# Kernel optimization log

Measured on AMD Instinct MI355X. Metric: run time of the kernel, lower is better.

Reference implementation:

```python
import jax, jax.numpy as jnp
import numpy as np

B, S, E, DQ, DV = 8, 2048, 1024, 128, 128


def setup_inputs() -> dict:
    k0 = jax.random.key(0)
    ks = jax.random.split(k0, 10)
    scale_in = 1.0 / np.sqrt(E)
    return {
        "pad_mask": jax.random.uniform(ks[0], (B, S)) < 0.1,  # True = padded key position
        "query": jax.random.normal(ks[1], (B, S, E), jnp.float32),
        "key": jax.random.normal(ks[2], (B, S, E), jnp.float32),
        "value": jax.random.normal(ks[3], (B, S, E), jnp.float32),
        "Wq": jax.random.uniform(ks[4], (E, DQ), jnp.float32, -scale_in, scale_in),
        "bq": jnp.zeros((DQ,), jnp.float32),
        "Wk": jax.random.uniform(ks[5], (E, DQ), jnp.float32, -scale_in, scale_in),
        "bk": jnp.zeros((DQ,), jnp.float32),
        "Wv": jax.random.uniform(ks[6], (E, DV), jnp.float32, -scale_in, scale_in),
        "bv": jnp.zeros((DV,), jnp.float32),
    }


def reference(pad_mask, query, key, value, Wq, bq, Wk, bk, Wv, bv):
    # Linear projections (torch Linear: x @ W^T + b; weights stored pre-transposed here)
    q = query @ Wq + bq  # [B,S,DQ]
    k = key @ Wk + bk    # [B,S,DQ]
    v = value @ Wv + bv  # [B,S,DV]

    scores = jnp.einsum("bqd,bkd->bqk", q, k)  # [B,S,S]
    # Causal mask applied BEFORE scaling (as in source); -inf/scale is still -inf
    seq = scores.shape[1]
    causal = jnp.triu(jnp.ones((seq, seq), bool), k=1)
    scores = jnp.where(causal[None], -jnp.inf, scores)
    scores = scores / jnp.asarray(q.shape[-1] ** 0.5, scores.dtype)
    # Padding mask: mask key positions with -1e9 (broadcast over query dim)
    scores = jnp.where(pad_mask[:, None, :], jnp.asarray(-1e9, scores.dtype), scores)

    attn = jax.nn.softmax(scores, axis=-1)
    return jnp.einsum("bqk,bkd->bqd", attn, v)  # [B,S,DV]
```

## Files before the change

### kernel.cpp

```cpp
#include <hip/hip_runtime.h>
#include <hip/hip_bf16.h>

#define SEQ 2048
#define EMB 1024
#define DH  128
#define QSCALE 0.08838834764831845f

typedef __attribute__((ext_vector_type(4))) float f32x4;
typedef __attribute__((ext_vector_type(8))) short bf16x8;
typedef __attribute__((ext_vector_type(4))) short bf16x4;

__device__ __forceinline__ short f2bf(float f) {
  unsigned u = __builtin_bit_cast(unsigned, f);
  u += 0x7fffu + ((u >> 16) & 1u);
  return (short)(u >> 16);
}

__device__ __forceinline__ float bf2f(short s) {
  unsigned u = ((unsigned)(unsigned short)s) << 16;
  return __builtin_bit_cast(float, u);
}

__device__ __forceinline__ f32x4 mfma16(bf16x8 a, bf16x8 b, f32x4 c) {
  return __builtin_amdgcn_mfma_f32_16x16x32_bf16(a, b, c, 0, 0, 0);
}

__device__ __forceinline__ void gl_lds16(void* lds_base, const void* gsrc) {
  __builtin_amdgcn_global_load_lds(
      (const __attribute__((address_space(1))) void*)gsrc,
      (__attribute__((address_space(3))) void*)lds_base, 16, 0, 0);
}

__global__ void prep_weights(const float* __restrict__ Wq, const float* __restrict__ Wk,
                             const float* __restrict__ Wv, short* __restrict__ wt) {
  int gid = blockIdx.x * 256 + threadIdx.x;
  int lane = gid & 63, c = lane & 15, g = (lane >> 4) & 3;
  int nb = (gid >> 6) & 7;
  int kk = (gid >> 9) & 31;
  int p = gid >> 14;
  const float* W = (p == 0) ? Wq : ((p == 1) ? Wk : Wv);
  bf16x8 v;
#pragma unroll
  for (int j = 0; j < 8; ++j)
    v[j] = f2bf(W[(kk * 32 + g * 8 + j) * DH + nb * 16 + c]);
  *(bf16x8*)(&wt[(size_t)gid * 8]) = v;
}

__global__ __launch_bounds__(256, 3) void proj_gemm(
    const float* __restrict__ Xq, const float* __restrict__ Xk, const float* __restrict__ Xv,
    const short* __restrict__ wt,
    const float* __restrict__ bq, const float* __restrict__ bk, const float* __restrict__ bv,
    short* __restrict__ qp, short* __restrict__ kp, short* __restrict__ vt) {
  const int tid = threadIdx.x;
  const int w = tid >> 6, lane = tid & 63;
  const int g = lane >> 4, c = lane & 15;
  const int p = blockIdx.x >> 8, mb = blockIdx.x & 255;
  const int row0 = (mb << 6) + (w << 4);
  const float* X    = (p == 0) ? Xq : ((p == 1) ? Xk : Xv);
  const float* bias = (p == 0) ? bq : ((p == 1) ? bk : bv);

  const f32x4* ap = (const f32x4*)(X + (size_t)(row0 + c) * 1024 + (g << 3));
  const bf16x8* wf = (const bf16x8*)(wt + ((size_t)p << 17)) + lane;

  f32x4 acc[8];
#pragma unroll
  for (int i = 0; i < 8; ++i) acc[i] = (f32x4){0.f, 0.f, 0.f, 0.f};

  f32x4 a0A, a1A, a0B, a1B;
  bf16x8 bA[8], bB[8];

  a0A = ap[0];
  a1A = ap[1];
#pragma unroll
  for (int nb = 0; nb < 8; ++nb) bA[nb] = wf[nb << 6];

#pragma unroll 1
  for (int kk = 0; kk < 32; kk += 2) {
    a0B = ap[(kk + 1) * 8];
    a1B = ap[(kk + 1) * 8 + 1];
#pragma unroll
    for (int nb = 0; nb < 8; ++nb) bB[nb] = wf[(kk + 1) * 512 + (nb << 6)];

    {
      bf16x8 a;
#pragma unroll
      for (int j = 0; j < 4; ++j) { a[j] = f2bf(a0A[j]); a[4 + j] = f2bf(a1A[j]); }
#pragma unroll
      for (int nb = 0; nb < 8; ++nb) acc[nb] = mfma16(a, bA[nb], acc[nb]);
    }

    if (kk + 2 < 32) {
      a0A = ap[(kk + 2) * 8];
      a1A = ap[(kk + 2) * 8 + 1];
#pragma unroll
      for (int nb = 0; nb < 8; ++nb) bA[nb] = wf[(kk + 2) * 512 + (nb << 6)];
    }

    {
      bf16x8 a;
#pragma unroll
      for (int j = 0; j < 4; ++j) { a[j] = f2bf(a0B[j]); a[4 + j] = f2bf(a1B[j]); }
#pragma unroll
      for (int nb = 0; nb < 8; ++nb) acc[nb] = mfma16(a, bB[nb], acc[nb]);
    }
  }

  float bvals[8];
#pragma unroll
  for (int nb = 0; nb < 8; ++nb) bvals[nb] = bias[nb * 16 + c];

  if (p < 2) {
    short* outp = (p == 0) ? qp : kp;
    float sc = (p == 0) ? QSCALE : 1.0f;
#pragma unroll
    for (int r = 0; r < 4; ++r) {
      int token = row0 + g * 4 + r;
#pragma unroll
      for (int nb = 0; nb < 8; ++nb)
        outp[token * 128 + nb * 16 + c] = f2bf((acc[nb][r] + bvals[nb]) * sc);
    }
  } else {
    int tok0 = row0 + g * 4;
    int b_ = tok0 >> 11, s_ = tok0 & 2047;
#pragma unroll
    for (int nb = 0; nb < 8; ++nb) {
      int col = nb * 16 + c;
      bf16x4 v4;
#pragma unroll
      for (int r = 0; r < 4; ++r) v4[r] = f2bf(acc[nb][r] + bvals[nb]);
      *(bf16x4*)(&vt[((size_t)(b_ * 128 + col)) * 2048 + s_]) = v4;
    }
  }
}

__global__ __launch_bounds__(256) void avgv2_kernel(
    const short* __restrict__ vt, const int* __restrict__ pad,
    const float* __restrict__ bvv, float* __restrict__ avgv) {
  int b = blockIdx.x >> 3, dg = blockIdx.x & 7;
  int t = threadIdx.x, doff = t >> 4, sl = t & 15;
  int d = dg * 16 + doff;
  const short* vrow = vt + ((size_t)(b * 128 + d)) * 2048 + sl * 128;
  const int* prow = pad + (b << 11) + sl * 128;
  float sum = 0.f;
  int cnt = 0;
  for (int i = 0; i < 16; ++i) {
    bf16x8 v8 = *(const bf16x8*)(vrow + i * 8);
#pragma unroll
    for (int j = 0; j < 8; ++j) {
      int pd = prow[i * 8 + j];
      cnt += (pd != 0);
      if (pd) sum += bf2f(v8[j]);
    }
  }
#pragma unroll
  for (int xm = 1; xm < 16; xm <<= 1) {
    sum += __shfl_xor(sum, xm, 64);
    cnt += __shfl_xor(cnt, xm, 64);
  }
  if (sl == 0) avgv[(b << 7) + d] = (cnt > 0) ? (sum / (float)cnt) : 0.f;
  (void)bvv;
}

__device__ __forceinline__ void stage_kv(short* kb, short* vb,
                                         const char* kb_base, const char* vb_base,
                                         int kt, int w, int lane) {
#pragma unroll
  for (int ch = w; ch < 16; ch += 4) {
    int phys = ch * 1024 + lane * 16;
    int lg = phys ^ (((phys >> 8) & 7) << 4);
    gl_lds16((char*)kb + ch * 1024,
             kb_base + (size_t)(kt * 64 + (lg >> 8)) * 256 + (lg & 255));
  }
#pragma unroll
  for (int ch = w; ch < 16; ch += 4) {
    int phys = ch * 1024 + lane * 16;
    int lg = phys ^ (((phys >> 7) & 7) << 4);
    gl_lds16((char*)vb + ch * 1024,
             vb_base + (size_t)(lg >> 7) * 4096 + kt * 128 + (lg & 127));
  }
}

template <bool CAUSAL>
__device__ __forceinline__ void attn_tile(
    const short* __restrict__ k_lds, const short* __restrict__ v_lds, short* __restrict__ p_w,
    const bf16x8 (&qf)[4], f32x4 (&acc_o)[8], float (&m_r)[4], float (&l_r)[4],
    const int* __restrict__ padp, int kt, int qrow_g, int g, int c) {
  f32x4 sc[4];
#pragma unroll
  for (int nb = 0; nb < 4; ++nb) sc[nb] = (f32x4){0.f, 0.f, 0.f, 0.f};
#pragma unroll
  for (int ks = 0; ks < 4; ++ks) {
    bf16x8 kf[4];
#pragma unroll
    for (int nb = 0; nb < 4; ++nb) {
      int n = (nb << 4) + c;
      int off = (n << 8) + (ks << 6) + (g << 4);
      kf[nb] = *(const bf16x8*)((const char*)k_lds + (off ^ ((n & 7) << 4)));
    }
#pragma unroll
    for (int nb = 0; nb < 4; ++nb) sc[nb] = mfma16(qf[ks], kf[nb], sc[nb]);
  }

  int padv[4];
#pragma unroll
  for (int nb = 0; nb < 4; ++nb) padv[nb] = padp[kt + (nb << 4) + c];
  float sv[4][4];
#pragma unroll
  for (int nb = 0; nb < 4; ++nb) {
    bool pd = padv[nb] != 0;
    int key = kt + (nb << 4) + c;
#pragma unroll
    for (int r = 0; r < 4; ++r) {
      float s = sc[nb][r];
      if (CAUSAL && key > qrow_g + r) s = -1e30f;
      if (pd) s = -1e30f;
      sv[nb][r] = s;
    }
  }
  float tmax[4];
#pragma unroll
  for (int r = 0; r < 4; ++r)
    tmax[r] = fmaxf(fmaxf(sv[0][r], sv[1][r]), fmaxf(sv[2][r], sv[3][r]));
#pragma unroll
  for (int xm = 1; xm < 16; xm <<= 1)
#pragma unroll
    for (int r = 0; r < 4; ++r) tmax[r] = fmaxf(tmax[r], __shfl_xor(tmax[r], xm, 64));
  float al[4];
#pragma unroll
  for (int r = 0; r < 4; ++r) {
    float mn = fmaxf(m_r[r], tmax[r]);
    al[r] = __expf(m_r[r] - mn);
    m_r[r] = mn;
  }
  float ls[4] = {0.f, 0.f, 0.f, 0.f};
#pragma unroll
  for (int nb = 0; nb < 4; ++nb)
#pragma unroll
    for (int r = 0; r < 4; ++r) {
      float pp = __expf(sv[nb][r] - m_r[r]);
      sv[nb][r] = pp;
      ls[r] += pp;
    }
#pragma unroll
  for (int xm = 1; xm < 16; xm <<= 1)
#pragma unroll
    for (int r = 0; r < 4; ++r) ls[r] += __shfl_xor(ls[r], xm, 64);
#pragma unroll
  for (int r = 0; r < 4; ++r) l_r[r] = l_r[r] * al[r] + ls[r];
#pragma unroll
  for (int nb = 0; nb < 8; ++nb)
#pragma unroll
    for (int r = 0; r < 4; ++r) acc_o[nb][r] *= al[r];

#pragma unroll
  for (int nb = 0; nb < 4; ++nb)
#pragma unroll
    for (int r = 0; r < 4; ++r)
      p_w[(g * 4 + r) * 72 + (nb << 4) + c] = f2bf(sv[nb][r]);

#pragma unroll
  for (int ks = 0; ks < 2; ++ks) {
    bf16x8 pa = *(const bf16x8*)((const char*)p_w + c * 144 + ks * 64 + g * 16);
#pragma unroll
    for (int nb = 0; nb < 8; ++nb) {
      int n = (nb << 4) + c;
      int off = (n << 7) + (ks << 6) + (g << 4);
      bf16x8 vf = *(const bf16x8*)((const char*)v_lds + (off ^ ((n & 7) << 4)));
      acc_o[nb] = mfma16(pa, vf, acc_o[nb]);
    }
  }
}

__global__ __launch_bounds__(256) void flash_attn(
    const short* __restrict__ qp, const short* __restrict__ kp, const short* __restrict__ vt,
    const int* __restrict__ pad, float* __restrict__ partO, float* __restrict__ partML) {
  __shared__ short k_lds[2][64 * 128];
  __shared__ short v_lds[2][128 * 64];
  __shared__ short p_lds[4][16 * 72];
  const int tid = threadIdx.x, w = tid >> 6, lane = tid & 63;
  const int g = lane >> 4, c = lane & 15;
  const int j = blockIdx.x;
  int b, qi, half;
  if (j < 256) { b = j >> 5; qi = j & 31; half = 0; }
  else { int u = j - 256; b = u >> 5; qi = 31 - (u & 31); half = 1; }
  const int T = qi + 1;
  const int t0 = half ? (T >> 1) : 0;
  const int t1 = half ? T : (T >> 1);
  const int q0 = qi << 6;

  bf16x8 qf[4];
  {
    int token = (b << 11) + q0 + (w << 4) + c;
    const char* qrow = (const char*)qp + (size_t)token * 256;
#pragma unroll
    for (int s = 0; s < 4; ++s) qf[s] = *(const bf16x8*)(qrow + s * 64 + g * 16);
  }
  f32x4 acc_o[8];
#pragma unroll
  for (int i = 0; i < 8; ++i) acc_o[i] = (f32x4){0.f, 0.f, 0.f, 0.f};
  float m_r[4] = {-1e30f, -1e30f, -1e30f, -1e30f};
  float l_r[4] = {0.f, 0.f, 0.f, 0.f};

  const char* kb_base = (const char*)kp + (size_t)(b << 11) * 256;
  const char* vb_base = (const char*)vt + (size_t)b * 524288;
  const int* padp = pad + (b << 11);
  const int qrow_g = q0 + (w << 4) + (g << 2);

  if (t1 > t0) {
    stage_kv(k_lds[0], v_lds[0], kb_base, vb_base, t0, w, lane);
    __syncthreads();
    int cur = 0;
    for (int t = t0; t < t1; ++t) {
      if (t + 1 < t1)
        stage_kv(k_lds[cur ^ 1], v_lds[cur ^ 1], kb_base, vb_base, t + 1, w, lane);
      if (half && t == T - 1)
        attn_tile<true>(k_lds[cur], v_lds[cur], p_lds[w], qf, acc_o, m_r, l_r,
                        padp, t << 6, qrow_g, g, c);
      else
        attn_tile<false>(k_lds[cur], v_lds[cur], p_lds[w], qf, acc_o, m_r, l_r,
                         padp, t << 6, qrow_g, g, c);
      __syncthreads();
      cur ^= 1;
    }
  }

  float* pO = partO + (size_t)j * (64 * 128);
  float* pML = partML + (size_t)j * 128;
#pragma unroll
  for (int nb = 0; nb < 8; ++nb)
#pragma unroll
    for (int r = 0; r < 4; ++r)
      pO[(w * 16 + g * 4 + r) * 128 + (nb << 4) + c] = acc_o[nb][r];
  if (c == 0)
#pragma unroll
    for (int r = 0; r < 4; ++r) {
      pML[(w * 16 + g * 4 + r) * 2] = m_r[r];
      pML[(w * 16 + g * 4 + r) * 2 + 1] = l_r[r];
    }
}

__global__ __launch_bounds__(256) void combine_kernel(
    const float* __restrict__ partO, const float* __restrict__ partML,
    const float* __restrict__ avgv, float* __restrict__ out) {
  int gid = blockIdx.x * 256 + threadIdx.x;
  int row = gid >> 5;
  int d4 = gid & 31;
  int b = row >> 11, s = row & 2047;
  int qt = s >> 6, lr = s & 63;
  int wid1 = (b << 5) + qt;
  int wid2 = 256 + (b << 5) + (31 - qt);
  float m1 = partML[wid1 * 128 + lr * 2], l1 = partML[wid1 * 128 + lr * 2 + 1];
  float m2 = partML[wid2 * 128 + lr * 2], l2 = partML[wid2 * 128 + lr * 2 + 1];
  float m = fmaxf(m1, m2);
  f32x4 o;
  if (m < -1e8f) {
    o = *(const f32x4*)(avgv + (b << 7) + (d4 << 2));
  } else {
    float f1 = __expf(m1 - m), f2 = __expf(m2 - m);
    float inv = 1.0f / (l1 * f1 + l2 * f2);
    f32x4 o1 = *(const f32x4*)(partO + ((size_t)wid1 * 64 + lr) * 128 + (d4 << 2));
    f32x4 o2 = *(const f32x4*)(partO + ((size_t)wid2 * 64 + lr) * 128 + (d4 << 2));
#pragma unroll
    for (int k = 0; k < 4; ++k) o[k] = (o1[k] * f1 + o2[k] * f2) * inv;
  }
  *(f32x4*)(out + (size_t)row * 128 + (d4 << 2)) = o;
}

extern "C" void kernel_launch(void* const* d_in, const int* in_sizes, int n_in,
                              void* d_out, int out_size, void* d_ws, size_t ws_size,
                              hipStream_t stream) {
  const int*   pad   = (const int*)d_in[0];
  const float* query = (const float*)d_in[1];
  const float* key   = (const float*)d_in[2];
  const float* value = (const float*)d_in[3];
  const float* Wq    = (const float*)d_in[4];
  const float* bq    = (const float*)d_in[5];
  const float* Wk    = (const float*)d_in[6];
  const float* bk    = (const float*)d_in[7];
  const float* Wv    = (const float*)d_in[8];
  const float* bv    = (const float*)d_in[9];
  char* ws = (char*)d_ws;
  short* wt    = (short*)ws;
  short* qp    = (short*)(ws + 786432);
  short* kp    = (short*)(ws + 4980736);
  short* vt    = (short*)(ws + 9175040);
  float* partO = (float*)(ws + 13369344);
  float* partML= (float*)(ws + 30146560);
  float* avgv  = (float*)(ws + 30408704);
  float* out   = (float*)d_out;

  prep_weights<<<dim3(192), dim3(256), 0, stream>>>(Wq, Wk, Wv, wt);
  proj_gemm<<<dim3(768), dim3(256), 0, stream>>>(query, key, value, wt, bq, bk, bv, qp, kp, vt);
  avgv2_kernel<<<dim3(64), dim3(256), 0, stream>>>(vt, pad, bv, avgv);
  flash_attn<<<dim3(512), dim3(256), 0, stream>>>(qp, kp, vt, pad, partO, partML);
  combine_kernel<<<dim3(2048), dim3(256), 0, stream>>>(partO, partML, avgv, out);
}
```

Before: 120.2 us.

## Restructure projection GEMM into single-wave blocks with double-buffered LDS staging

The projection GEMM now runs one 64-thread wave per block, and each wave computes 32 rows instead of 16. Activation and weight tiles are staged with direct global-to-LDS loads into a double buffer, using an XOR swizzle to avoid bank conflicts, and explicit vmcnt waits overlap the next tile's load with the current tile's MFMAs. Each weight fragment is now reused across two row blocks, which halves weight traffic per row. The cost is more LDS per block and more accumulator registers, plus reliance on hand-placed waitcnt counts for correctness.

```diff
diff --git a/kernel.cpp b/kernel.cpp
--- a/kernel.cpp
+++ b/kernel.cpp
@@ -46,63 +46,77 @@
   *(bf16x8*)(&wt[(size_t)gid * 8]) = v;
 }
 
-__global__ __launch_bounds__(256, 3) void proj_gemm(
+__global__ __launch_bounds__(64, 2) void proj_gemm(
     const float* __restrict__ Xq, const float* __restrict__ Xk, const float* __restrict__ Xv,
     const short* __restrict__ wt,
     const float* __restrict__ bq, const float* __restrict__ bk, const float* __restrict__ bv,
     short* __restrict__ qp, short* __restrict__ kp, short* __restrict__ vt) {
-  const int tid = threadIdx.x;
-  const int w = tid >> 6, lane = tid & 63;
+  __shared__ char abuf[2][4096];
+  __shared__ char wbuf[2][8192];
+
+  const int lane = threadIdx.x;
   const int g = lane >> 4, c = lane & 15;
-  const int p = blockIdx.x >> 8, mb = blockIdx.x & 255;
-  const int row0 = (mb << 6) + (w << 4);
+  const int wid = blockIdx.x;
+  const int p = wid >> 9, mb = wid & 511;
+  const int row0 = mb << 5;
   const float* X    = (p == 0) ? Xq : ((p == 1) ? Xk : Xv);
   const float* bias = (p == 0) ? bq : ((p == 1) ? bk : bv);
-
-  const f32x4* ap = (const f32x4*)(X + (size_t)(row0 + c) * 1024 + (g << 3));
-  const bf16x8* wf = (const bf16x8*)(wt + ((size_t)p << 17)) + lane;
-
-  f32x4 acc[8];
-#pragma unroll
-  for (int i = 0; i < 8; ++i) acc[i] = (f32x4){0.f, 0.f, 0.f, 0.f};
-
-  f32x4 a0A, a1A, a0B, a1B;
-  bf16x8 bA[8], bB[8];
-
-  a0A = ap[0];
-  a1A = ap[1];
-#pragma unroll
-  for (int nb = 0; nb < 8; ++nb) bA[nb] = wf[nb << 6];
-
+  const char* Xb  = (const char*)X;
+  const char* Wtb = (const char*)wt + (size_t)p * 262144;
+
+  f32x4 acc[2][8];
+#pragma unroll
+  for (int rb = 0; rb < 2; ++rb)
+#pragma unroll
+    for (int nb = 0; nb < 8; ++nb) acc[rb][nb] = (f32x4){0.f, 0.f, 0.f, 0.f};
+
+  auto stage = [&](char* ab, char* wb, int kk) {
+#pragma unroll
+    for (int i = 0; i < 4; ++i) {
+      int q = i * 1024 + lane * 16;
+      int lg = q ^ (((q >> 7) & 7) << 4);
+      gl_lds16(ab + i * 1024,
+               Xb + (size_t)(row0 + (lg >> 7)) * 4096 + kk * 128 + (lg & 127));
+    }
+#pragma unroll
+    for (int i = 0; i < 8; ++i)
+      gl_lds16(wb + i * 1024, Wtb + (size_t)kk * 8192 + i * 1024 + lane * 16);
+  };
+
+  auto compute = [&](const char* ab, const char* wb) {
+    bf16x8 wfr[8];
+#pragma unroll
+    for (int nb = 0; nb < 8; ++nb)
+      wfr[nb] = *(const bf16x8*)(wb + nb * 1024 + lane * 16);
+#pragma unroll
+    for (int rb = 0; rb < 2; ++rb) {
+      int r = (rb << 4) + c;
+      int ad = ((r << 7) + (g << 5)) ^ ((r & 7) << 4);
+      f32x4 lo = *(const f32x4*)(ab + ad);
+      f32x4 hi = *(const f32x4*)(ab + (ad ^ 16));
+      bf16x8 a;
+#pragma unroll
+      for (int j = 0; j < 4; ++j) { a[j] = f2bf(lo[j]); a[4 + j] = f2bf(hi[j]); }
+#pragma unroll
+      for (int nb = 0; nb < 8; ++nb) acc[rb][nb] = mfma16(a, wfr[nb], acc[rb][nb]);
+    }
+  };
+
+  stage(abuf[0], wbuf[0], 0);
 #pragma unroll 1
   for (int kk = 0; kk < 32; kk += 2) {
-    a0B = ap[(kk + 1) * 8];
-    a1B = ap[(kk + 1) * 8 + 1];
-#pragma unroll
-    for (int nb = 0; nb < 8; ++nb) bB[nb] = wf[(kk + 1) * 512 + (nb << 6)];
-
-    {
-      bf16x8 a;
-#pragma unroll
-      for (int j = 0; j < 4; ++j) { a[j] = f2bf(a0A[j]); a[4 + j] = f2bf(a1A[j]); }
-#pragma unroll
-      for (int nb = 0; nb < 8; ++nb) acc[nb] = mfma16(a, bA[nb], acc[nb]);
-    }
-
+    stage(abuf[1], wbuf[1], kk + 1);
+    asm volatile("s_waitcnt vmcnt(12)" ::: "memory");
+    compute(abuf[0], wbuf[0]);
+    __builtin_amdgcn_sched_barrier(0);
     if (kk + 2 < 32) {
-      a0A = ap[(kk + 2) * 8];
-      a1A = ap[(kk + 2) * 8 + 1];
-#pragma unroll
-      for (int nb = 0; nb < 8; ++nb) bA[nb] = wf[(kk + 2) * 512 + (nb << 6)];
-    }
-
-    {
-      bf16x8 a;
-#pragma unroll
-      for (int j = 0; j < 4; ++j) { a[j] = f2bf(a0B[j]); a[4 + j] = f2bf(a1B[j]); }
-#pragma unroll
-      for (int nb = 0; nb < 8; ++nb) acc[nb] = mfma16(a, bB[nb], acc[nb]);
-    }
+      stage(abuf[0], wbuf[0], kk + 2);
+      asm volatile("s_waitcnt vmcnt(12)" ::: "memory");
+    } else {
+      asm volatile("s_waitcnt vmcnt(0)" ::: "memory");
+    }
+    compute(abuf[1], wbuf[1]);
+    __builtin_amdgcn_sched_barrier(0);
   }
 
   float bvals[8];
@@ -113,22 +127,27 @@
     short* outp = (p == 0) ? qp : kp;
     float sc = (p == 0) ? QSCALE : 1.0f;
 #pragma unroll
-    for (int r = 0; r < 4; ++r) {
-      int token = row0 + g * 4 + r;
-#pragma unroll
-      for (int nb = 0; nb < 8; ++nb)
-        outp[token * 128 + nb * 16 + c] = f2bf((acc[nb][r] + bvals[nb]) * sc);
-    }
+    for (int rb = 0; rb < 2; ++rb)
+#pragma unroll
+      for (int r = 0; r < 4; ++r) {
+        int token = row0 + (rb << 4) + g * 4 + r;
+#pragma unroll
+        for (int nb = 0; nb < 8; ++nb)
+          outp[token * 128 + nb * 16 + c] = f2bf((acc[rb][nb][r] + bvals[nb]) * sc);
+      }
   } else {
-    int tok0 = row0 + g * 4;
-    int b_ = tok0 >> 11, s_ = tok0 & 2047;
-#pragma unroll
-    for (int nb = 0; nb < 8; ++nb) {
-      int col = nb * 16 + c;
-      bf16x4 v4;
-#pragma unroll
-      for (int r = 0; r < 4; ++r) v4[r] = f2bf(acc[nb][r] + bvals[nb]);
-      *(bf16x4*)(&vt[((size_t)(b_ * 128 + col)) * 2048 + s_]) = v4;
+#pragma unroll
+    for (int rb = 0; rb < 2; ++rb) {
+      int tok0 = row0 + (rb << 4) + g * 4;
+      int b_ = tok0 >> 11, s_ = tok0 & 2047;
+#pragma unroll
+      for (int nb = 0; nb < 8; ++nb) {
+        int col = nb * 16 + c;
+        bf16x4 v4;
+#pragma unroll
+        for (int r = 0; r < 4; ++r) v4[r] = f2bf(acc[rb][nb][r] + bvals[nb]);
+        *(bf16x4*)(&vt[((size_t)(b_ * 128 + col)) * 2048 + s_]) = v4;
+      }
     }
   }
 }
@@ -390,7 +409,7 @@
   float* out   = (float*)d_out;
 
   prep_weights<<<dim3(192), dim3(256), 0, stream>>>(Wq, Wk, Wv, wt);
-  proj_gemm<<<dim3(768), dim3(256), 0, stream>>>(query, key, value, wt, bq, bk, bv, qp, kp, vt);
+  proj_gemm<<<dim3(1536), dim3(64), 0, stream>>>(query, key, value, wt, bq, bk, bv, qp, kp, vt);
   avgv2_kernel<<<dim3(64), dim3(256), 0, stream>>>(vt, pad, bv, avgv);
   flash_attn<<<dim3(512), dim3(256), 0, stream>>>(qp, kp, vt, pad, partO, partML);
   combine_kernel<<<dim3(2048), dim3(256), 0, stream>>>(partO, partML, avgv, out);
```

Result: faster. 97.60 us (-18.8%).

## Stage projection GEMM tiles through LDS with triple-buffered async loads

Applied to the files above, without the earlier changes.

The projection GEMM now loads activation and weight tiles into shared memory with direct global-to-LDS copies (gl_lds16). Loads are triple-buffered and gated by vmcnt waits and barriers; the old path used per-wave register double-buffering straight from global memory. Activation tiles use an XOR-swizzled layout to avoid LDS bank conflicts, and each block starts its K loop at a different rotated offset to spread memory traffic. This shares weight tiles across the four waves and overlaps loads with MFMA, at the cost of 48KB of LDS per block and a barrier every iteration, which may lower occupancy.

```diff
diff --git a/kernel.cpp b/kernel.cpp
--- a/kernel.cpp
+++ b/kernel.cpp
@@ -51,58 +51,75 @@
     const short* __restrict__ wt,
     const float* __restrict__ bq, const float* __restrict__ bk, const float* __restrict__ bv,
     short* __restrict__ qp, short* __restrict__ kp, short* __restrict__ vt) {
+  __shared__ char abuf[3][8192];
+  __shared__ char wbuf[3][8192];
+
   const int tid = threadIdx.x;
   const int w = tid >> 6, lane = tid & 63;
   const int g = lane >> 4, c = lane & 15;
-  const int p = blockIdx.x >> 8, mb = blockIdx.x & 255;
-  const int row0 = (mb << 6) + (w << 4);
+  const int bid = blockIdx.x;
+  const int p = bid >> 8, mb = bid & 255;
+  const int row0 = mb << 6;
+  const int k0 = (bid * 5) & 31;
   const float* X    = (p == 0) ? Xq : ((p == 1) ? Xk : Xv);
   const float* bias = (p == 0) ? bq : ((p == 1) ? bk : bv);
-
-  const f32x4* ap = (const f32x4*)(X + (size_t)(row0 + c) * 1024 + (g << 3));
-  const bf16x8* wf = (const bf16x8*)(wt + ((size_t)p << 17)) + lane;
+  const char* Xb  = (const char*)X;
+  const char* Wtb = (const char*)wt + (size_t)p * 262144;
 
   f32x4 acc[8];
 #pragma unroll
-  for (int i = 0; i < 8; ++i) acc[i] = (f32x4){0.f, 0.f, 0.f, 0.f};
-
-  f32x4 a0A, a1A, a0B, a1B;
-  bf16x8 bA[8], bB[8];
-
-  a0A = ap[0];
-  a1A = ap[1];
-#pragma unroll
-  for (int nb = 0; nb < 8; ++nb) bA[nb] = wf[nb << 6];
-
+  for (int nb = 0; nb < 8; ++nb) acc[nb] = (f32x4){0.f, 0.f, 0.f, 0.f};
+
+  auto stage = [&](int buf, int kk) {
+#pragma unroll
+    for (int i = 0; i < 2; ++i) {
+      int ch = w + i * 4;
+      int phys = ch * 1024 + lane * 16;
+      int lg = phys ^ (((phys >> 7) & 7) << 4);
+      gl_lds16(abuf[buf] + ch * 1024,
+               Xb + (size_t)(row0 + (lg >> 7)) * 4096 + kk * 128 + (lg & 127));
+    }
+#pragma unroll
+    for (int i = 0; i < 2; ++i) {
+      int ch = w + i * 4;
+      gl_lds16(wbuf[buf] + ch * 1024,
+               Wtb + (size_t)kk * 8192 + ch * 1024 + lane * 16);
+    }
+  };
+
+  auto compute = [&](int buf) {
+    const char* ab = abuf[buf];
+    const char* wb = wbuf[buf];
+    bf16x8 wfr[8];
+#pragma unroll
+    for (int nb = 0; nb < 8; ++nb)
+      wfr[nb] = *(const bf16x8*)(wb + nb * 1024 + lane * 16);
+    int r = (w << 4) + c;
+    int ad = (r << 7) + ((g << 5) ^ ((r & 7) << 4));
+    f32x4 lo = *(const f32x4*)(ab + ad);
+    f32x4 hi = *(const f32x4*)(ab + (ad ^ 16));
+    bf16x8 a;
+#pragma unroll
+    for (int j = 0; j < 4; ++j) { a[j] = f2bf(lo[j]); a[4 + j] = f2bf(hi[j]); }
+#pragma unroll
+    for (int nb = 0; nb < 8; ++nb) acc[nb] = mfma16(a, wfr[nb], acc[nb]);
+  };
+
+  stage(0, k0);
+  int bufc = 0;
 #pragma unroll 1
-  for (int kk = 0; kk < 32; kk += 2) {
-    a0B = ap[(kk + 1) * 8];
-    a1B = ap[(kk + 1) * 8 + 1];
-#pragma unroll
-    for (int nb = 0; nb < 8; ++nb) bB[nb] = wf[(kk + 1) * 512 + (nb << 6)];
-
-    {
-      bf16x8 a;
-#pragma unroll
-      for (int j = 0; j < 4; ++j) { a[j] = f2bf(a0A[j]); a[4 + j] = f2bf(a1A[j]); }
-#pragma unroll
-      for (int nb = 0; nb < 8; ++nb) acc[nb] = mfma16(a, bA[nb], acc[nb]);
-    }
-
-    if (kk + 2 < 32) {
-      a0A = ap[(kk + 2) * 8];
-      a1A = ap[(kk + 2) * 8 + 1];
-#pragma unroll
-      for (int nb = 0; nb < 8; ++nb) bA[nb] = wf[(kk + 2) * 512 + (nb << 6)];
-    }
-
-    {
-      bf16x8 a;
-#pragma unroll
-      for (int j = 0; j < 4; ++j) { a[j] = f2bf(a0B[j]); a[4 + j] = f2bf(a1B[j]); }
-#pragma unroll
-      for (int nb = 0; nb < 8; ++nb) acc[nb] = mfma16(a, bB[nb], acc[nb]);
-    }
+  for (int t = 0; t < 32; ++t) {
+    int nbuf = (bufc == 2) ? 0 : bufc + 1;
+    if (t + 1 < 32) {
+      stage(nbuf, (k0 + t + 1) & 31);
+      asm volatile("s_waitcnt vmcnt(4)" ::: "memory");
+    } else {
+      asm volatile("s_waitcnt vmcnt(0)" ::: "memory");
+    }
+    __builtin_amdgcn_s_barrier();
+    __builtin_amdgcn_sched_barrier(0);
+    compute(bufc);
+    bufc = nbuf;
   }
 
   float bvals[8];
@@ -114,13 +131,13 @@
     float sc = (p == 0) ? QSCALE : 1.0f;
 #pragma unroll
     for (int r = 0; r < 4; ++r) {
-      int token = row0 + g * 4 + r;
+      int token = row0 + (w << 4) + g * 4 + r;
 #pragma unroll
       for (int nb = 0; nb < 8; ++nb)
         outp[token * 128 + nb * 16 + c] = f2bf((acc[nb][r] + bvals[nb]) * sc);
     }
   } else {
-    int tok0 = row0 + g * 4;
+    int tok0 = row0 + (w << 4) + g * 4;
     int b_ = tok0 >> 11, s_ = tok0 & 2047;
 #pragma unroll
     for (int nb = 0; nb < 8; ++nb) {
```

Measured after the change: 96.80 us, median of 2. 19.4% less time.

## Stage projection A tiles through LDS with async copies and manual vmcnt pipelining

Applied to the files above, without the earlier changes.

Rewrites the projection GEMM main loop so each wave streams its fp32 activation rows into a per-wave double-buffered LDS region using direct global-to-LDS 16-byte loads, with an XOR swizzle to avoid bank conflicts. Weight fragments are double-buffered in registers, and explicit s_waitcnt counts plus sched_barriers control how loads overlap with MFMA work. The goal is wider coalesced global reads of X and deeper prefetch than the previous per-lane strided loads. In exchange it uses 64KB of LDS per block, lowers launch bounds to 2 blocks per CU, and depends on hand-counted vmcnt values being correct.

```diff
diff --git a/kernel.cpp b/kernel.cpp
--- a/kernel.cpp
+++ b/kernel.cpp
@@ -46,63 +46,74 @@
   *(bf16x8*)(&wt[(size_t)gid * 8]) = v;
 }
 
-__global__ __launch_bounds__(256, 3) void proj_gemm(
+__global__ __launch_bounds__(256, 2) void proj_gemm(
     const float* __restrict__ Xq, const float* __restrict__ Xk, const float* __restrict__ Xv,
     const short* __restrict__ wt,
     const float* __restrict__ bq, const float* __restrict__ bk, const float* __restrict__ bv,
     short* __restrict__ qp, short* __restrict__ kp, short* __restrict__ vt) {
+  __shared__ char a_lds[4][2][8192];
+
   const int tid = threadIdx.x;
   const int w = tid >> 6, lane = tid & 63;
   const int g = lane >> 4, c = lane & 15;
-  const int p = blockIdx.x >> 8, mb = blockIdx.x & 255;
+  const int bid = blockIdx.x;
+  const int p = bid >> 8, mb = bid & 255;
   const int row0 = (mb << 6) + (w << 4);
   const float* X    = (p == 0) ? Xq : ((p == 1) ? Xk : Xv);
   const float* bias = (p == 0) ? bq : ((p == 1) ? bk : bv);
-
-  const f32x4* ap = (const f32x4*)(X + (size_t)(row0 + c) * 1024 + (g << 3));
-  const bf16x8* wf = (const bf16x8*)(wt + ((size_t)p << 17)) + lane;
+  const char* Xs  = (const char*)X + (size_t)row0 * 4096;
+  const char* WT  = (const char*)wt + (size_t)p * 262144;
 
   f32x4 acc[8];
 #pragma unroll
-  for (int i = 0; i < 8; ++i) acc[i] = (f32x4){0.f, 0.f, 0.f, 0.f};
-
-  f32x4 a0A, a1A, a0B, a1B;
-  bf16x8 bA[8], bB[8];
-
-  a0A = ap[0];
-  a1A = ap[1];
-#pragma unroll
-  for (int nb = 0; nb < 8; ++nb) bA[nb] = wf[nb << 6];
-
-#pragma unroll 1
-  for (int kk = 0; kk < 32; kk += 2) {
-    a0B = ap[(kk + 1) * 8];
-    a1B = ap[(kk + 1) * 8 + 1];
-#pragma unroll
-    for (int nb = 0; nb < 8; ++nb) bB[nb] = wf[(kk + 1) * 512 + (nb << 6)];
-
-    {
-      bf16x8 a;
-#pragma unroll
-      for (int j = 0; j < 4; ++j) { a[j] = f2bf(a0A[j]); a[4 + j] = f2bf(a1A[j]); }
-#pragma unroll
-      for (int nb = 0; nb < 8; ++nb) acc[nb] = mfma16(a, bA[nb], acc[nb]);
-    }
-
-    if (kk + 2 < 32) {
-      a0A = ap[(kk + 2) * 8];
-      a1A = ap[(kk + 2) * 8 + 1];
-#pragma unroll
-      for (int nb = 0; nb < 8; ++nb) bA[nb] = wf[(kk + 2) * 512 + (nb << 6)];
-    }
-
-    {
-      bf16x8 a;
-#pragma unroll
-      for (int j = 0; j < 4; ++j) { a[j] = f2bf(a0B[j]); a[4 + j] = f2bf(a1B[j]); }
-#pragma unroll
-      for (int nb = 0; nb < 8; ++nb) acc[nb] = mfma16(a, bB[nb], acc[nb]);
-    }
+  for (int nb = 0; nb < 8; ++nb) acc[nb] = (f32x4){0.f, 0.f, 0.f, 0.f};
+
+  bf16x8 wr[2][8];
+
+  auto stage_A = [&](int b, int kc) {
+#pragma unroll
+    for (int j = 0; j < 8; ++j) {
+      int r = (j << 1) + (lane >> 5);
+      int off = ((lane & 31) << 4) ^ ((r & 7) << 5);
+      gl_lds16(&a_lds[w][b][j * 1024],
+               Xs + (size_t)r * 4096 + kc * 512 + off);
+    }
+  };
+
+  auto loadW = [&](bf16x8* dst, int t) {
+#pragma unroll
+    for (int nb = 0; nb < 8; ++nb)
+      dst[nb] = *(const bf16x8*)(WT + (size_t)t * 8192 + nb * 1024 + (lane << 4));
+  };
+
+  auto computeT = [&](const bf16x8* wf, int b, int s) {
+    const char* ab = &a_lds[w][b][0];
+    int ad = (c << 9) + (((s << 7) + (g << 5)) ^ ((c & 7) << 5));
+    f32x4 lo = *(const f32x4*)(ab + ad);
+    f32x4 hi = *(const f32x4*)(ab + ad + 16);
+    bf16x8 a;
+#pragma unroll
+    for (int j = 0; j < 4; ++j) { a[j] = f2bf(lo[j]); a[4 + j] = f2bf(hi[j]); }
+#pragma unroll
+    for (int nb = 0; nb < 8; ++nb) acc[nb] = mfma16(a, wf[nb], acc[nb]);
+  };
+
+  stage_A(0, 0);
+  loadW(wr[0], 0);
+  __builtin_amdgcn_sched_barrier(0);
+
+#pragma unroll
+  for (int t = 0; t < 32; ++t) {
+    const int s = t & 3, kc = t >> 2;
+    if (s == 0 && kc < 7) stage_A((kc + 1) & 1, kc + 1);
+    if (t + 1 < 32) loadW(wr[(t + 1) & 1], t + 1);
+    __builtin_amdgcn_sched_barrier(0);
+    if (t == 31)                       asm volatile("s_waitcnt vmcnt(0)" ::: "memory");
+    else if (s == 0 && t <= 24)        asm volatile("s_waitcnt vmcnt(16)" ::: "memory");
+    else                               asm volatile("s_waitcnt vmcnt(8)" ::: "memory");
+    __builtin_amdgcn_sched_barrier(0);
+    computeT(wr[t & 1], kc & 1, s);
+    __builtin_amdgcn_sched_barrier(0);
   }
 
   float bvals[8];
```

Result: faster. 105.6 us (-12.2%).
